# Optimization experiments

Measured on AMD Instinct MI355X. Metric: run time of the kernel, lower is better.

## Reference

```python
import jax, jax.numpy as jnp
import numpy as np

RATIO = 0.2  # init ratio


def setup_inputs() -> dict:
    key = jax.random.key(0)
    inputs = jax.random.normal(key, (8, 19, 512, 1024), dtype=jnp.float32)
    return {"inputs": inputs}


def reference(inputs):
    # inputs: (N, C, H, W) logits
    N, C, H, W = inputs.shape
    p = jax.nn.softmax(inputs, axis=1)          # applySoftMax=True
    argpred = jnp.argmax(p, axis=1)              # (N, H, W)

    def image_weight(ap):
        # histogram of predicted classes over C bins (histc with min=0, max=C-1)
        h = jnp.zeros((C,), jnp.float32).at[ap.reshape(-1)].add(1.0)
        h = jnp.where(h == 0.0, 1.0, h)          # hist[hist==0] = 1
        return (h.sum() / h) ** RATIO            # (C,)

    weights = jax.vmap(image_weight)(argpred)    # (N, C), detached in original
    weights = jax.lax.stop_gradient(weights)

    loss = -(p ** 2) * weights[:, :, None, None]  # (N, C, H, W)
    return loss.mean()                            # reduction='mean'
```

## Files before the change

kernel.cpp:

```cpp
#include <hip/hip_runtime.h>

#define N_IMG 8
#define C_CLS 19
#define H_DIM 512
#define W_DIM 1024
#define HW (H_DIM * W_DIM)
#define HW4 (HW / 4)
#define TOTAL_ELEMS (N_IMG * C_CLS * HW)
#define RATIO 0.2f

#define BLOCKS_X 512
#define BLOCK_THREADS 256

__device__ __forceinline__ float& f4c(float4& v, int k) {
    return reinterpret_cast<float*>(&v)[k];
}

__global__ __launch_bounds__(BLOCK_THREADS, 4) void iw_pass1(
    const float* __restrict__ in,
    float* __restrict__ Q,
    int* __restrict__ Hist)
{
    const int n = blockIdx.y;
    const float4* base4 = reinterpret_cast<const float4*>(in + (size_t)n * C_CLS * HW);
    const int i = blockIdx.x * BLOCK_THREADS + threadIdx.x;

    float4 x4[C_CLS];
#pragma unroll
    for (int c = 0; c < C_CLS; ++c)
        x4[c] = base4[(size_t)c * HW4 + i];

    float q[C_CLS];
#pragma unroll
    for (int c = 0; c < C_CLS; ++c) q[c] = 0.0f;

    int hw_cnt[C_CLS];
#pragma unroll
    for (int c = 0; c < C_CLS; ++c) hw_cnt[c] = 0;

#pragma unroll
    for (int k = 0; k < 4; ++k) {
        float m = f4c(x4[0], k);
        int   am = 0;
#pragma unroll
        for (int c = 1; c < C_CLS; ++c) {
            float xc = f4c(x4[c], k);
            if (xc > m) { m = xc; am = c; }
        }
#pragma unroll
        for (int c = 0; c < C_CLS; ++c)
            hw_cnt[c] += (int)__popcll(__ballot(am == c));

        float S = 0.0f;
#pragma unroll
        for (int c = 0; c < C_CLS; ++c) {
            float e = __expf(f4c(x4[c], k) - m);
            S += e;
            f4c(x4[c], k) = e * e;
        }
        float inv = 1.0f / (S * S);
#pragma unroll
        for (int c = 0; c < C_CLS; ++c)
            q[c] = fmaf(f4c(x4[c], k), inv, q[c]);
    }

#pragma unroll
    for (int c = 0; c < C_CLS; ++c) {
        float v = q[c];
#pragma unroll
        for (int off = 32; off > 0; off >>= 1)
            v += __shfl_xor(v, off, 64);
        q[c] = v;
    }

    __shared__ float qs[4 * C_CLS];
    __shared__ int   hs[4 * C_CLS];
    const int tid = threadIdx.x;
    const int wave = tid >> 6, lane = tid & 63;
    if (lane == 0) {
#pragma unroll
        for (int c = 0; c < C_CLS; ++c) {
            qs[wave * C_CLS + c] = q[c];
            hs[wave * C_CLS + c] = hw_cnt[c];
        }
    }
    __syncthreads();
    if (tid < C_CLS) {
        float s  = qs[tid] + qs[C_CLS + tid] + qs[2 * C_CLS + tid] + qs[3 * C_CLS + tid];
        int   hv = hs[tid] + hs[C_CLS + tid] + hs[2 * C_CLS + tid] + hs[3 * C_CLS + tid];
        atomicAdd(&Q[n * C_CLS + tid], s);
        atomicAdd(&Hist[n * C_CLS + tid], hv);
    }
}

__global__ __launch_bounds__(64) void iw_pass2(
    const float* __restrict__ Q,
    const int* __restrict__ Hist,
    float* __restrict__ out)
{
    const int t = threadIdx.x;
    float loss = 0.0f;
    if (t < N_IMG) {
        float h[C_CLS];
        float hs = 0.0f;
#pragma unroll
        for (int c = 0; c < C_CLS; ++c) {
            float v = (float)Hist[t * C_CLS + c];
            v = (v == 0.0f) ? 1.0f : v;
            h[c] = v;
            hs += v;
        }
#pragma unroll
        for (int c = 0; c < C_CLS; ++c) {
            float w = powf(hs / h[c], RATIO);
            loss = fmaf(w, Q[t * C_CLS + c], loss);
        }
    }
    loss += __shfl_xor(loss, 1, 64);
    loss += __shfl_xor(loss, 2, 64);
    loss += __shfl_xor(loss, 4, 64);
    if (t == 0)
        out[0] = -loss / (float)TOTAL_ELEMS;
}

extern "C" void kernel_launch(void* const* d_in, const int* in_sizes, int n_in,
                              void* d_out, int out_size, void* d_ws, size_t ws_size,
                              hipStream_t stream)
{
    const float* in = (const float*)d_in[0];
    float* out = (float*)d_out;

    float* Q  = (float*)d_ws;
    int* Hist = (int*)((char*)d_ws + N_IMG * C_CLS * sizeof(float));

    hipMemsetAsync(d_ws, 0, N_IMG * C_CLS * (sizeof(float) + sizeof(int)), stream);

    dim3 grid(BLOCKS_X, N_IMG);
    iw_pass1<<<grid, BLOCK_THREADS, 0, stream>>>(in, Q, Hist);
    iw_pass2<<<1, 64, 0, stream>>>(Q, Hist, out);
}
```

Measured before the change: 422.1 us.

## Double-buffer float2 loads across four strided iterations per thread

Each thread now processes four strided chunks of two pixels using float2 loads, with two register buffers so the next chunk's 19 loads are in flight while the current one is computed. The grid shrinks to half as many blocks, so each block covers more pixels and there are fewer atomics and reductions per element. It aims to overlap memory latency with compute inside a thread, at the cost of the same register footprint (two float2 buffers instead of one float4 buffer) and fewer waves in flight.

```diff
diff --git a/kernel.cpp b/kernel.cpp
--- a/kernel.cpp
+++ b/kernel.cpp
@@ -5,15 +5,52 @@
 #define H_DIM 512
 #define W_DIM 1024
 #define HW (H_DIM * W_DIM)
-#define HW4 (HW / 4)
+#define HW2 (HW / 2)
 #define TOTAL_ELEMS (N_IMG * C_CLS * HW)
 #define RATIO 0.2f
 
-#define BLOCKS_X 512
+#define BLOCKS_X 256
 #define BLOCK_THREADS 256
+#define STRIDE (BLOCKS_X * BLOCK_THREADS)
+#define ITERS 4
 
-__device__ __forceinline__ float& f4c(float4& v, int k) {
+__device__ __forceinline__ float& f2c(float2& v, int k) {
     return reinterpret_cast<float*>(&v)[k];
+}
+
+__device__ __forceinline__ void load19(const float2* __restrict__ base2, int idx,
+                                       float2 (&x)[C_CLS]) {
+#pragma unroll
+    for (int c = 0; c < C_CLS; ++c)
+        x[c] = base2[(size_t)c * HW2 + idx];
+}
+
+__device__ __forceinline__ void compute19(float2 (&x)[C_CLS], float (&q)[C_CLS],
+                                          int (&hw_cnt)[C_CLS]) {
+#pragma unroll
+    for (int k = 0; k < 2; ++k) {
+        float m = f2c(x[0], k);
+        int   am = 0;
+#pragma unroll
+        for (int c = 1; c < C_CLS; ++c) {
+            float xc = f2c(x[c], k);
+            if (xc > m) { m = xc; am = c; }
+        }
+#pragma unroll
+        for (int c = 0; c < C_CLS; ++c)
+            hw_cnt[c] += (int)__popcll(__ballot(am == c));
+        float S = 0.0f;
+#pragma unroll
+        for (int c = 0; c < C_CLS; ++c) {
+            float e = __expf(f2c(x[c], k) - m);
+            S += e;
+            f2c(x[c], k) = e * e;
+        }
+        float inv = 1.0f / (S * S);
+#pragma unroll
+        for (int c = 0; c < C_CLS; ++c)
+            q[c] = fmaf(f2c(x[c], k), inv, q[c]);
+    }
 }
 
 __global__ __launch_bounds__(BLOCK_THREADS, 4) void iw_pass1(
@@ -22,47 +59,25 @@
     int* __restrict__ Hist)
 {
     const int n = blockIdx.y;
-    const float4* base4 = reinterpret_cast<const float4*>(in + (size_t)n * C_CLS * HW);
-    const int i = blockIdx.x * BLOCK_THREADS + threadIdx.x;
-
-    float4 x4[C_CLS];
-#pragma unroll
-    for (int c = 0; c < C_CLS; ++c)
-        x4[c] = base4[(size_t)c * HW4 + i];
+    const float2* base2 = reinterpret_cast<const float2*>(in + (size_t)n * C_CLS * HW);
+    const int i0 = blockIdx.x * BLOCK_THREADS + threadIdx.x;
 
     float q[C_CLS];
 #pragma unroll
     for (int c = 0; c < C_CLS; ++c) q[c] = 0.0f;
-
     int hw_cnt[C_CLS];
 #pragma unroll
     for (int c = 0; c < C_CLS; ++c) hw_cnt[c] = 0;
 
-#pragma unroll
-    for (int k = 0; k < 4; ++k) {
-        float m = f4c(x4[0], k);
-        int   am = 0;
-#pragma unroll
-        for (int c = 1; c < C_CLS; ++c) {
-            float xc = f4c(x4[c], k);
-            if (xc > m) { m = xc; am = c; }
-        }
-#pragma unroll
-        for (int c = 0; c < C_CLS; ++c)
-            hw_cnt[c] += (int)__popcll(__ballot(am == c));
-
-        float S = 0.0f;
-#pragma unroll
-        for (int c = 0; c < C_CLS; ++c) {
-            float e = __expf(f4c(x4[c], k) - m);
-            S += e;
-            f4c(x4[c], k) = e * e;
-        }
-        float inv = 1.0f / (S * S);
-#pragma unroll
-        for (int c = 0; c < C_CLS; ++c)
-            q[c] = fmaf(f4c(x4[c], k), inv, q[c]);
-    }
+    float2 A[C_CLS], B[C_CLS];
+    load19(base2, i0,              A);
+    load19(base2, i0 + 1 * STRIDE, B);
+    compute19(A, q, hw_cnt);
+    load19(base2, i0 + 2 * STRIDE, A);
+    compute19(B, q, hw_cnt);
+    load19(base2, i0 + 3 * STRIDE, B);
+    compute19(A, q, hw_cnt);
+    compute19(B, q, hw_cnt);
 
 #pragma unroll
     for (int c = 0; c < C_CLS; ++c) {
```

Measured after the change: 427.9 us. About the same (+1.4%).
